# Kernel tuning notes

Measured on AMD Instinct MI355X. Metric: run time of the kernel, lower is better.

Reference implementation:

```python
import jax, jax.numpy as jnp
import numpy as np

N, E, S = 10000, 100000, 10            # nodes, edges, message-passing steps
NODE_F, EDGE_F, L, H, OUT = 30, 4, 128, 128, 3


def _mlp(h, W0, b0, W1, b1, W2, b2):
    # Linear->ReLU, Linear->ReLU, Linear (build_mlp with num_hidden_layers=2)
    h = jax.nn.relu(h @ W0 + b0)
    h = jax.nn.relu(h @ W1 + b1)
    return h @ W2 + b2


def _ln(h, g, b):
    # torch.nn.LayerNorm over last dim, eps=1e-5, biased variance
    m = h.mean(-1, keepdims=True)
    v = h.var(-1, keepdims=True)
    return (h - m) * jax.lax.rsqrt(v + 1e-5) * g + b


def setup_inputs():
    key = jax.random.key(0)
    ks = iter(jax.random.split(key, 64))

    def w(shape, fan):
        return jax.random.normal(next(ks), shape, dtype=jnp.float32) / np.float32(np.sqrt(fan))

    d = {}
    d["x"] = jax.random.normal(next(ks), (N, NODE_F), dtype=jnp.float32)
    d["ea"] = jax.random.normal(next(ks), (E, EDGE_F), dtype=jnp.float32)
    d["ei"] = jax.random.randint(next(ks), (2, E), 0, N)
    # encoder node ('en') / edge ('ee') MLP+LayerNorm params
    for pre, fin in (("en", NODE_F), ("ee", EDGE_F)):
        d[pre + "W0"] = w((fin, H), fin); d[pre + "b0"] = jnp.zeros((H,), jnp.float32)
        d[pre + "W1"] = w((H, H), H);     d[pre + "b1"] = jnp.zeros((H,), jnp.float32)
        d[pre + "W2"] = w((H, L), H);     d[pre + "b2"] = jnp.zeros((L,), jnp.float32)
        d[pre + "g"] = jnp.ones((L,), jnp.float32); d[pre + "bt"] = jnp.zeros((L,), jnp.float32)
    # processor edge ('pe', in=3L) / node ('pn', in=2L) params, stacked over S steps
    for pre, fin in (("pe", 3 * L), ("pn", 2 * L)):
        d[pre + "W0"] = w((S, fin, H), fin); d[pre + "b0"] = jnp.zeros((S, H), jnp.float32)
        d[pre + "W1"] = w((S, H, H), H);     d[pre + "b1"] = jnp.zeros((S, H), jnp.float32)
        d[pre + "W2"] = w((S, H, L), H);     d[pre + "b2"] = jnp.zeros((S, L), jnp.float32)
        d[pre + "g"] = jnp.ones((S, L), jnp.float32); d[pre + "bt"] = jnp.zeros((S, L), jnp.float32)
    # decoder MLP (no LayerNorm)
    d["dW0"] = w((L, H), L); d["db0"] = jnp.zeros((H,), jnp.float32)
    d["dW1"] = w((H, H), H); d["db1"] = jnp.zeros((H,), jnp.float32)
    d["dW2"] = w((H, OUT), H); d["db2"] = jnp.zeros((OUT,), jnp.float32)
    return d


def reference(x, ea, ei,
              enW0, enb0, enW1, enb1, enW2, enb2, eng, enbt,
              eeW0, eeb0, eeW1, eeb1, eeW2, eeb2, eeg, eebt,
              peW0, peb0, peW1, peb1, peW2, peb2, peg, pebt,
              pnW0, pnb0, pnW1, pnb1, pnW2, pnb2, png, pnbt,
              dW0, db0, dW1, db1, dW2, db2):
    src, dst = ei[0], ei[1]
    # encode (GraphIndependent)
    hx = _ln(_mlp(x, enW0, enb0, enW1, enb1, enW2, enb2), eng, enbt)   # [N, L]
    he = _ln(_mlp(ea, eeW0, eeb0, eeW1, eeb1, eeW2, eeb2), eeg, eebt)  # [E, L]

    # process: S InteractionNetwork steps with residuals
    def step(carry, p):
        cx, ce = carry
        (eW0, eb0, eW1, eb1, eW2, eb2, eg, ebt,
         nW0, nb0, nW1, nb1, nW2, nb2, ng, nbt) = p
        edge_in = jnp.concatenate([cx[src], cx[dst], ce], axis=-1)     # [E, 3L]
        ue = _ln(_mlp(edge_in, eW0, eb0, eW1, eb1, eW2, eb2), eg, ebt)  # [E, L]
        agg = jax.ops.segment_sum(ue, dst, num_segments=N)              # [N, L]
        un = _ln(_mlp(jnp.concatenate([cx, agg], axis=-1), nW0, nb0, nW1, nb1, nW2, nb2), ng, nbt)
        return (cx + un, ce + ue), None

    (hx, he), _ = jax.lax.scan(
        step, (hx, he),
        (peW0, peb0, peW1, peb1, peW2, peb2, peg, pebt,
         pnW0, pnb0, pnW1, pnb1, pnW2, pnb2, png, pnbt))

    # decode
    return _mlp(hx, dW0, db0, dW1, db1, dW2, db2)  # [N, OUT]
```

## Files before the change

### kernel.cpp

```cpp
#include <hip/hip_runtime.h>


#define NN 10000
#define NE 100000
#define STEPS 10
#define NODE_F 30
#define EDGE_F 4
#define L 128
#define AP 132
#define BP 36

#define WS_STRIDE 136
#define AB_STRIDE 136

typedef __bf16 bf16x8 __attribute__((ext_vector_type(8)));
typedef float f32x4 __attribute__((ext_vector_type(4)));

__device__ __forceinline__ unsigned short f2bf(float f) {
  __bf16 b = (__bf16)f;
  return __builtin_bit_cast(unsigned short, b);
}
__device__ __forceinline__ float bf2f(unsigned short u) {
  return __builtin_bit_cast(float, (unsigned)u << 16);
}


__device__ __forceinline__ void stage_W(unsigned short* __restrict__ Ws,
                                        const unsigned short* __restrict__ Wt,
                                        int K, int sec, int tid) {
#pragma unroll
  for (int p = 0; p < 8; ++p) {
    int u = tid + p * 256;
    int n = u >> 4, kk = u & 15;
    uint4 v = *(const uint4*)(Wt + (size_t)n * K + sec * 128 + kk * 8);
    *(uint4*)&Ws[n * WS_STRIDE + kk * 8] = v;
  }
}

__device__ __forceinline__ void init_acc(f32x4 acc[2][4], const float* __restrict__ b,
                                         int wcol, int l16) {
#pragma unroll
  for (int j = 0; j < 4; ++j) {
    float bv = b[wcol + j * 16 + l16];
#pragma unroll
    for (int i = 0; i < 2; ++i) acc[i][j] = f32x4{bv, bv, bv, bv};
  }
}

__device__ __forceinline__ void layer_gbf(const unsigned short* __restrict__ ap0,
                                          const unsigned short* __restrict__ ap1,
                                          const unsigned short* __restrict__ Ws,
                                          f32x4 acc[2][4], int wcol, int l4, int l16) {
#pragma unroll
  for (int kk = 0; kk < 4; ++kk) {
    bf16x8 af[2];
    af[0] = *(const bf16x8*)(ap0 + kk * 32 + l4 * 8);
    af[1] = *(const bf16x8*)(ap1 + kk * 32 + l4 * 8);
#pragma unroll
    for (int j = 0; j < 4; ++j) {
      bf16x8 bv = *(const bf16x8*)&Ws[(wcol + j * 16 + l16) * WS_STRIDE + kk * 32 + l4 * 8];
#pragma unroll
      for (int i = 0; i < 2; ++i)
        acc[i][j] = __builtin_amdgcn_mfma_f32_16x16x32_bf16(af[i], bv, acc[i][j], 0, 0, 0);
    }
  }
}

__device__ __forceinline__ void layer_lds(const unsigned short* __restrict__ Ab,
                                          const unsigned short* __restrict__ Ws,
                                          f32x4 acc[2][4], int wrow, int wcol, int l4, int l16) {
#pragma unroll
  for (int kk = 0; kk < 4; ++kk) {
    bf16x8 af[2];
#pragma unroll
    for (int i = 0; i < 2; ++i)
      af[i] = *(const bf16x8*)&Ab[(wrow + i * 16 + l16) * AB_STRIDE + kk * 32 + l4 * 8];
#pragma unroll
    for (int j = 0; j < 4; ++j) {
      bf16x8 bv = *(const bf16x8*)&Ws[(wcol + j * 16 + l16) * WS_STRIDE + kk * 32 + l4 * 8];
#pragma unroll
      for (int i = 0; i < 2; ++i)
        acc[i][j] = __builtin_amdgcn_mfma_f32_16x16x32_bf16(af[i], bv, acc[i][j], 0, 0, 0);
    }
  }
}

__device__ __forceinline__ void relu_to_Ab(unsigned short* __restrict__ Ab, f32x4 acc[2][4],
                                           int wrow, int wcol, int l4, int l16) {
#pragma unroll
  for (int i = 0; i < 2; ++i)
#pragma unroll
    for (int j = 0; j < 4; ++j)
#pragma unroll
      for (int r = 0; r < 4; ++r) {
        int row = wrow + i * 16 + l4 * 4 + r;
        int col = wcol + j * 16 + l16;
        __bf16 v = (__bf16)fmaxf(acc[i][j][r], 0.f);
        Ab[row * AB_STRIDE + col] = __builtin_bit_cast(unsigned short, v);
      }
}

__device__ __forceinline__ void ln_partials(const f32x4 acc[2][4], float ps[2][4], float ps2[2][4]) {
#pragma unroll
  for (int i = 0; i < 2; ++i)
#pragma unroll
    for (int r = 0; r < 4; ++r) {
      float s = 0.f, s2 = 0.f;
#pragma unroll
      for (int j = 0; j < 4; ++j) { float v = acc[i][j][r]; s += v; s2 += v * v; }
#pragma unroll
      for (int off = 1; off < 16; off <<= 1) {
        s += __shfl_xor(s, off, 64);
        s2 += __shfl_xor(s2, off, 64);
      }
      ps[i][r] = s; ps2[i][r] = s2;
    }
}


__global__ __launch_bounds__(256) void deg_kernel(const int* __restrict__ ei, int* __restrict__ cnt) {
  int e = blockIdx.x * 256 + threadIdx.x;
  if (e < NE) atomicAdd(&cnt[ei[NE + e]], 1);
}

__global__ __launch_bounds__(256) void scan_kernel(const int* __restrict__ cnt,
                                                   int* __restrict__ off, int* __restrict__ cur) {
  __shared__ int sums[256];
  int t = threadIdx.x;
  int base = t * 40;
  int local = 0;
  for (int i = 0; i < 40; ++i) { int n = base + i; if (n < NN) local += cnt[n]; }
  sums[t] = local;
  __syncthreads();
  int val = local;
  for (int d = 1; d < 256; d <<= 1) {
    int add = (t >= d) ? sums[t - d] : 0;
    __syncthreads();
    sums[t] += add;
    __syncthreads();
  }
  int run = sums[t] - val;
  for (int i = 0; i < 40; ++i) {
    int n = base + i;
    if (n < NN) { off[n] = run; cur[n] = run; run += cnt[n]; }
  }
  if (t == 255) off[NN] = sums[255];
}

__global__ __launch_bounds__(256) void scatter_kernel(const int* __restrict__ ei,
                                                      int* __restrict__ cur, int* __restrict__ eid) {
  int e = blockIdx.x * 256 + threadIdx.x;
  if (e < NE) { int p = atomicAdd(&cur[ei[NE + e]], 1); eid[p] = e; }
}

__global__ __launch_bounds__(256) void agg_kernel(const unsigned short* __restrict__ ue,
                                                  const int* __restrict__ off,
                                                  const int* __restrict__ eid,
                                                  unsigned short* __restrict__ agg) {
  int node = blockIdx.x * 4 + (threadIdx.x >> 6);
  if (node >= NN) return;
  int lane = threadIdx.x & 63;
  int c0 = lane * 2;
  int p0 = off[node], p1 = off[node + 1];
  float sx = 0.f, sy = 0.f;
  for (int p = p0; p < p1; ++p) {
    unsigned v = *(const unsigned*)&ue[(size_t)eid[p] * L + c0];
    sx += __builtin_bit_cast(float, v << 16);
    sy += __builtin_bit_cast(float, v & 0xffff0000u);
  }
  unsigned o = (unsigned)f2bf(sx) | ((unsigned)f2bf(sy) << 16);
  *(unsigned*)&agg[(size_t)node * L + c0] = o;
}


__global__ __launch_bounds__(256) void edge_step_mfma(
    const unsigned short* __restrict__ hx_bf, unsigned short* __restrict__ he_bf,
    unsigned short* __restrict__ ue_bf,
    const int* __restrict__ ei,
    const unsigned short* __restrict__ W0t, const float* __restrict__ b0,
    const unsigned short* __restrict__ W1t, const float* __restrict__ b1,
    const unsigned short* __restrict__ W2t, const float* __restrict__ b2,
    const float* __restrict__ g, const float* __restrict__ bt) {
  __shared__ __align__(16) unsigned short Ws[128 * WS_STRIDE];
  __shared__ __align__(16) unsigned short Ab[64 * AB_STRIDE];
  __shared__ int sidx[64], didx[64];
  int tid = threadIdx.x;
  int w = tid >> 6, lane = tid & 63;
  int l4 = lane >> 4, l16 = lane & 15;
  int wrow = (w >> 1) * 32, wcol = (w & 1) * 64;
  int e0 = blockIdx.x * 64;
  if (tid < 64) {
    int e = min(e0 + tid, NE - 1);
    sidx[tid] = ei[e];
    didx[tid] = ei[NE + e];
  }
  f32x4 acc[2][4];
  init_acc(acc, b0, wcol, l16);
  __syncthreads();
  for (int sec = 0; sec < 3; ++sec) {
    stage_W(Ws, W0t, 384, sec, tid);
    const unsigned short* ap[2];
#pragma unroll
    for (int i = 0; i < 2; ++i) {
      int r = wrow + i * 16 + l16;
      if (sec == 0)      ap[i] = hx_bf + (size_t)sidx[r] * L;
      else if (sec == 1) ap[i] = hx_bf + (size_t)didx[r] * L;
      else               ap[i] = he_bf + (size_t)min(e0 + r, NE - 1) * L;
    }
    __syncthreads();
    layer_gbf(ap[0], ap[1], Ws, acc, wcol, l4, l16);
    __syncthreads();
  }
  relu_to_Ab(Ab, acc, wrow, wcol, l4, l16);
  stage_W(Ws, W1t, 128, 0, tid);
  init_acc(acc, b1, wcol, l16);
  __syncthreads();
  layer_lds(Ab, Ws, acc, wrow, wcol, l4, l16);
  __syncthreads();
  relu_to_Ab(Ab, acc, wrow, wcol, l4, l16);
  stage_W(Ws, W2t, 128, 0, tid);
  init_acc(acc, b2, wcol, l16);
  __syncthreads();
  layer_lds(Ab, Ws, acc, wrow, wcol, l4, l16);
  float ps[2][4], ps2[2][4];
  ln_partials(acc, ps, ps2);
  __syncthreads();
  float* red = (float*)Ab;
  if (l16 == 0) {
#pragma unroll
    for (int i = 0; i < 2; ++i)
#pragma unroll
      for (int r = 0; r < 4; ++r) {
        int row = wrow + i * 16 + l4 * 4 + r;
        red[(w & 1) * 128 + row * 2 + 0] = ps[i][r];
        red[(w & 1) * 128 + row * 2 + 1] = ps2[i][r];
      }
  }
  __syncthreads();
  float gv[4], btv[4];
#pragma unroll
  for (int j = 0; j < 4; ++j) {
    int col = wcol + j * 16 + l16;
    gv[j] = g[col]; btv[j] = bt[col];
  }
#pragma unroll
  for (int i = 0; i < 2; ++i)
#pragma unroll
    for (int r = 0; r < 4; ++r) {
      int row = wrow + i * 16 + l4 * 4 + r;
      float s  = red[row * 2]     + red[128 + row * 2];
      float s2 = red[row * 2 + 1] + red[128 + row * 2 + 1];
      float m = s * (1.f / 128.f);
      float inv = rsqrtf(s2 * (1.f / 128.f) - m * m + 1e-5f);
      int e = e0 + row;
      if (e < NE) {
        size_t hoff = (size_t)e * L;
#pragma unroll
        for (int j = 0; j < 4; ++j) {
          int col = wcol + j * 16 + l16;
          float u = (acc[i][j][r] - m) * inv * gv[j] + btv[j];
          unsigned short old = he_bf[hoff + col];
          he_bf[hoff + col] = f2bf(bf2f(old) + u);
          ue_bf[hoff + col] = f2bf(u);
        }
      }
    }
}

__global__ __launch_bounds__(256) void node_step_mfma(
    float* __restrict__ hx, unsigned short* __restrict__ hx_bf,
    const unsigned short* __restrict__ agg_bf,
    const unsigned short* __restrict__ W0t, const float* __restrict__ b0,
    const unsigned short* __restrict__ W1t, const float* __restrict__ b1,
    const unsigned short* __restrict__ W2t, const float* __restrict__ b2,
    const float* __restrict__ g, const float* __restrict__ bt) {
  __shared__ __align__(16) unsigned short Ws[128 * WS_STRIDE];
  __shared__ __align__(16) unsigned short Ab[64 * AB_STRIDE];
  int tid = threadIdx.x;
  int w = tid >> 6, lane = tid & 63;
  int l4 = lane >> 4, l16 = lane & 15;
  int wrow = (w >> 1) * 32, wcol = (w & 1) * 64;
  int n0 = blockIdx.x * 64;
  f32x4 acc[2][4];
  init_acc(acc, b0, wcol, l16);
  for (int sec = 0; sec < 2; ++sec) {
    __syncthreads();
    stage_W(Ws, W0t, 256, sec, tid);
    const unsigned short* base = (sec == 0) ? hx_bf : agg_bf;
    const unsigned short* ap[2];
#pragma unroll
    for (int i = 0; i < 2; ++i)
      ap[i] = base + (size_t)min(n0 + wrow + i * 16 + l16, NN - 1) * L;
    __syncthreads();
    layer_gbf(ap[0], ap[1], Ws, acc, wcol, l4, l16);
  }
  __syncthreads();
  relu_to_Ab(Ab, acc, wrow, wcol, l4, l16);
  stage_W(Ws, W1t, 128, 0, tid);
  init_acc(acc, b1, wcol, l16);
  __syncthreads();
  layer_lds(Ab, Ws, acc, wrow, wcol, l4, l16);
  __syncthreads();
  relu_to_Ab(Ab, acc, wrow, wcol, l4, l16);
  stage_W(Ws, W2t, 128, 0, tid);
  init_acc(acc, b2, wcol, l16);
  __syncthreads();
  layer_lds(Ab, Ws, acc, wrow, wcol, l4, l16);
  float ps[2][4], ps2[2][4];
  ln_partials(acc, ps, ps2);
  __syncthreads();
  float* red = (float*)Ab;
  if (l16 == 0) {
#pragma unroll
    for (int i = 0; i < 2; ++i)
#pragma unroll
      for (int r = 0; r < 4; ++r) {
        int row = wrow + i * 16 + l4 * 4 + r;
        red[(w & 1) * 128 + row * 2 + 0] = ps[i][r];
        red[(w & 1) * 128 + row * 2 + 1] = ps2[i][r];
      }
  }
  __syncthreads();
  float gv[4], btv[4];
#pragma unroll
  for (int j = 0; j < 4; ++j) {
    int col = wcol + j * 16 + l16;
    gv[j] = g[col]; btv[j] = bt[col];
  }
#pragma unroll
  for (int i = 0; i < 2; ++i)
#pragma unroll
    for (int r = 0; r < 4; ++r) {
      int row = wrow + i * 16 + l4 * 4 + r;
      float s  = red[row * 2]     + red[128 + row * 2];
      float s2 = red[row * 2 + 1] + red[128 + row * 2 + 1];
      float m = s * (1.f / 128.f);
      float inv = rsqrtf(s2 * (1.f / 128.f) - m * m + 1e-5f);
      int n = n0 + row;
      if (n < NN) {
#pragma unroll
        for (int j = 0; j < 4; ++j) {
          int col = wcol + j * 16 + l16;
          float un = (acc[i][j][r] - m) * inv * gv[j] + btv[j];
          float nv = hx[(size_t)n * L + col] + un;
          hx[(size_t)n * L + col] = nv;
          hx_bf[(size_t)n * L + col] = f2bf(nv);
        }
      }
    }
}

__global__ __launch_bounds__(256) void enc_edge_mfma(
    const float* __restrict__ ea,
    const float* __restrict__ W0, const float* __restrict__ b0,
    const unsigned short* __restrict__ W1t, const float* __restrict__ b1,
    const unsigned short* __restrict__ W2t, const float* __restrict__ b2,
    const float* __restrict__ g, const float* __restrict__ bt,
    unsigned short* __restrict__ he_bf) {
  __shared__ __align__(16) unsigned short Ws[128 * WS_STRIDE];
  __shared__ __align__(16) unsigned short Ab[64 * AB_STRIDE];
  int tid = threadIdx.x;
  int w = tid >> 6, lane = tid & 63;
  int l4 = lane >> 4, l16 = lane & 15;
  int wrow = (w >> 1) * 32, wcol = (w & 1) * 64;
  int e0 = blockIdx.x * 64;
  {
    int row = tid >> 2, cbase = (tid & 3) * 32;
    int e = min(e0 + row, NE - 1);
    float4 eav = *(const float4*)&ea[(size_t)e * 4];
#pragma unroll
    for (int c = 0; c < 32; ++c) {
      int col = cbase + c;
      float sum = b0[col] + eav.x * W0[col] + eav.y * W0[128 + col] +
                  eav.z * W0[256 + col] + eav.w * W0[384 + col];
      __bf16 v = (__bf16)fmaxf(sum, 0.f);
      Ab[row * AB_STRIDE + col] = __builtin_bit_cast(unsigned short, v);
    }
  }
  stage_W(Ws, W1t, 128, 0, tid);
  f32x4 acc[2][4];
  init_acc(acc, b1, wcol, l16);
  __syncthreads();
  layer_lds(Ab, Ws, acc, wrow, wcol, l4, l16);
  __syncthreads();
  relu_to_Ab(Ab, acc, wrow, wcol, l4, l16);
  stage_W(Ws, W2t, 128, 0, tid);
  init_acc(acc, b2, wcol, l16);
  __syncthreads();
  layer_lds(Ab, Ws, acc, wrow, wcol, l4, l16);
  float ps[2][4], ps2[2][4];
  ln_partials(acc, ps, ps2);
  __syncthreads();
  float* red = (float*)Ab;
  if (l16 == 0) {
#pragma unroll
    for (int i = 0; i < 2; ++i)
#pragma unroll
      for (int r = 0; r < 4; ++r) {
        int row = wrow + i * 16 + l4 * 4 + r;
        red[(w & 1) * 128 + row * 2 + 0] = ps[i][r];
        red[(w & 1) * 128 + row * 2 + 1] = ps2[i][r];
      }
  }
  __syncthreads();
  float gv[4], btv[4];
#pragma unroll
  for (int j = 0; j < 4; ++j) {
    int col = wcol + j * 16 + l16;
    gv[j] = g[col]; btv[j] = bt[col];
  }
#pragma unroll
  for (int i = 0; i < 2; ++i)
#pragma unroll
    for (int r = 0; r < 4; ++r) {
      int row = wrow + i * 16 + l4 * 4 + r;
      float s  = red[row * 2]     + red[128 + row * 2];
      float s2 = red[row * 2 + 1] + red[128 + row * 2 + 1];
      float m = s * (1.f / 128.f);
      float inv = rsqrtf(s2 * (1.f / 128.f) - m * m + 1e-5f);
      int e = e0 + row;
      if (e < NE) {
#pragma unroll
        for (int j = 0; j < 4; ++j) {
          int col = wcol + j * 16 + l16;
          he_bf[(size_t)e * L + col] = f2bf((acc[i][j][r] - m) * inv * gv[j] + btv[j]);
        }
      }
    }
}


__global__ __launch_bounds__(256) void wprep_kernel(
    const float* __restrict__ W0, const float* __restrict__ W1, const float* __restrict__ W2,
    unsigned short* __restrict__ out, int K0, int steps) {
  int per_step = 128 * (K0 + 256);
  int idx = blockIdx.x * 256 + threadIdx.x;
  if (idx >= steps * per_step) return;
  int s = idx / per_step, r = idx - s * per_step;
  float v;
  if (r < 128 * K0) {
    int n = r / K0, k = r - n * K0;
    v = W0[(size_t)s * K0 * 128 + (size_t)k * 128 + n];
  } else {
    r -= 128 * K0;
    const float* W = (r < 16384) ? W1 : W2;
    r &= 16383;
    int n = r >> 7, k = r & 127;
    v = W[(size_t)s * 16384 + k * 128 + n];
  }
  out[idx] = f2bf(v);
}

__global__ __launch_bounds__(256) void tprep_kernel(
    const float* __restrict__ W1, const float* __restrict__ W2, unsigned short* __restrict__ out) {
  int idx = blockIdx.x * 256 + threadIdx.x;
  const float* W = (idx < 16384) ? W1 : W2;
  int r = idx & 16383;
  int n = r >> 7, k = r & 127;
  out[idx] = f2bf(W[k * 128 + n]);
}


__device__ __forceinline__ void load_B(float* __restrict__ Bs, const float* __restrict__ W,
                                       int K, int k0, int tid) {
#pragma unroll
  for (int p = 0; p < 16; ++p) {
    int idx = tid + p * 256;
    int kk = idx >> 7;
    int c = idx & 127;
    float v = 0.f;
    if (k0 + kk < K) v = W[(size_t)(k0 + kk) * L + c];
    Bs[c * BP + kk] = v;
  }
}

__device__ __forceinline__ void fma32(const float* __restrict__ As, const float* __restrict__ Bs,
                                      float acc[4][8], int ty, int tx, int koff) {
#pragma unroll
  for (int kk = 0; kk < 32; kk += 4) {
    float4 a[4];
    float4 b[8];
#pragma unroll
    for (int i = 0; i < 4; ++i)
      a[i] = *(const float4*)&As[(ty + 16 * i) * AP + koff + kk];
#pragma unroll
    for (int j = 0; j < 8; ++j)
      b[j] = *(const float4*)&Bs[(tx + 16 * j) * BP + kk];
#pragma unroll
    for (int i = 0; i < 4; ++i)
#pragma unroll
      for (int j = 0; j < 8; ++j) {
        acc[i][j] = fmaf(a[i].x, b[j].x, acc[i][j]);
        acc[i][j] = fmaf(a[i].y, b[j].y, acc[i][j]);
        acc[i][j] = fmaf(a[i].z, b[j].z, acc[i][j]);
        acc[i][j] = fmaf(a[i].w, b[j].w, acc[i][j]);
      }
  }
}

__device__ __forceinline__ void init_bias(float acc[4][8], const float* __restrict__ b, int tx) {
#pragma unroll
  for (int j = 0; j < 8; ++j) {
    float bv = b[tx + 16 * j];
#pragma unroll
    for (int i = 0; i < 4; ++i) acc[i][j] = bv;
  }
}

__device__ __forceinline__ void store_relu(float* __restrict__ As, float acc[4][8], int ty, int tx) {
#pragma unroll
  for (int i = 0; i < 4; ++i)
#pragma unroll
    for (int j = 0; j < 8; ++j)
      As[(ty + 16 * i) * AP + tx + 16 * j] = fmaxf(acc[i][j], 0.f);
}

__device__ __forceinline__ void layer_As(const float* __restrict__ As, float* __restrict__ Bs,
                                         const float* __restrict__ W, const float* __restrict__ bias,
                                         int K, float acc[4][8], int tid, int ty, int tx) {
  init_bias(acc, bias, tx);
  int nc = (K + 31) >> 5;
  for (int bc = 0; bc < nc; ++bc) {
    __syncthreads();
    load_B(Bs, W, K, bc * 32, tid);
    __syncthreads();
    fma32(As, Bs, acc, ty, tx, bc * 32);
  }
}

__device__ __forceinline__ void fillA_gather(float* __restrict__ As, const float* __restrict__ base,
                                             const int* __restrict__ ridx, int tid) {
#pragma unroll
  for (int p = 0; p < 8; ++p) {
    int idx = tid + p * 256;
    int r = idx >> 5;
    int c4 = idx & 31;
    float4 v = *(const float4*)&base[(size_t)ridx[r] * L + c4 * 4];
    *(float4*)&As[r * AP + c4 * 4] = v;
  }
}

__device__ __forceinline__ void lnorm(float acc[4][8], const float* __restrict__ g,
                                      const float* __restrict__ bt, int tx) {
  float gv[8], bv[8];
#pragma unroll
  for (int j = 0; j < 8; ++j) { gv[j] = g[tx + 16 * j]; bv[j] = bt[tx + 16 * j]; }
#pragma unroll
  for (int i = 0; i < 4; ++i) {
    float s = 0.f, s2 = 0.f;
#pragma unroll
    for (int j = 0; j < 8; ++j) { s += acc[i][j]; s2 += acc[i][j] * acc[i][j]; }
#pragma unroll
    for (int off = 1; off < 16; off <<= 1) {
      s  += __shfl_xor(s, off, 64);
      s2 += __shfl_xor(s2, off, 64);
    }
    float m = s * (1.f / 128.f);
    float var = s2 * (1.f / 128.f) - m * m;
    float inv = rsqrtf(var + 1e-5f);
#pragma unroll
    for (int j = 0; j < 8; ++j) acc[i][j] = (acc[i][j] - m) * inv * gv[j] + bv[j];
  }
}

__global__ __launch_bounds__(256) void enc_node_kernel(
    const float* __restrict__ x,
    const float* __restrict__ W0, const float* __restrict__ b0,
    const float* __restrict__ W1, const float* __restrict__ b1,
    const float* __restrict__ W2, const float* __restrict__ b2,
    const float* __restrict__ g, const float* __restrict__ bt,
    float* __restrict__ hx, unsigned short* __restrict__ hx_bf) {
  __shared__ float As[64 * AP];
  __shared__ float Bs[128 * BP];
  int tid = threadIdx.x, ty = tid >> 4, tx = tid & 15;
  int n0 = blockIdx.x * 64;
#pragma unroll
  for (int p = 0; p < 8; ++p) {
    int idx = tid + p * 256;
    int r = idx >> 5, c = idx & 31;
    int n = min(n0 + r, NN - 1);
    As[r * AP + c] = (c < NODE_F) ? x[(size_t)n * NODE_F + c] : 0.f;
  }
  float acc[4][8];
  init_bias(acc, b0, tx);
  __syncthreads();
  load_B(Bs, W0, NODE_F, 0, tid);
  __syncthreads();
  fma32(As, Bs, acc, ty, tx, 0);

  __syncthreads(); store_relu(As, acc, ty, tx);
  layer_As(As, Bs, W1, b1, L, acc, tid, ty, tx);
  __syncthreads(); store_relu(As, acc, ty, tx);
  layer_As(As, Bs, W2, b2, L, acc, tid, ty, tx);
  lnorm(acc, g, bt, tx);
#pragma unroll
  for (int i = 0; i < 4; ++i) {
    int n = n0 + ty + 16 * i;
    if (n < NN)
#pragma unroll
      for (int j = 0; j < 8; ++j) {
        float v = acc[i][j];
        hx[(size_t)n * L + tx + 16 * j] = v;
        hx_bf[(size_t)n * L + tx + 16 * j] = f2bf(v);
      }
  }
}

__global__ __launch_bounds__(256) void dec_kernel(
    const float* __restrict__ hx,
    const float* __restrict__ W0, const float* __restrict__ b0,
    const float* __restrict__ W1, const float* __restrict__ b1,
    const float* __restrict__ W2, const float* __restrict__ b2,
    float* __restrict__ out) {
  __shared__ float As[64 * AP];
  __shared__ float Bs[128 * BP];
  __shared__ int nidx[64];
  int tid = threadIdx.x, ty = tid >> 4, tx = tid & 15;
  int n0 = blockIdx.x * 64;
  if (tid < 64) nidx[tid] = min(n0 + tid, NN - 1);
  __syncthreads();
  fillA_gather(As, hx, nidx, tid);
  float acc[4][8];
  layer_As(As, Bs, W0, b0, L, acc, tid, ty, tx);
  __syncthreads(); store_relu(As, acc, ty, tx);
  layer_As(As, Bs, W1, b1, L, acc, tid, ty, tx);
  __syncthreads(); store_relu(As, acc, ty, tx);
  __syncthreads();
  if (tid < 192) {
    int r = tid / 3, o = tid - (tid / 3) * 3;
    int n = n0 + r;
    if (n < NN) {
      float s = b2[o];
#pragma unroll 8
      for (int k = 0; k < L; ++k) s = fmaf(As[r * AP + k], W2[k * 3 + o], s);
      out[(size_t)n * 3 + o] = s;
    }
  }
}


extern "C" void kernel_launch(void* const* d_in, const int* in_sizes, int n_in,
                              void* d_out, int out_size, void* d_ws, size_t ws_size,
                              hipStream_t stream) {
  (void)in_sizes; (void)n_in; (void)out_size; (void)ws_size;
  const float* x    = (const float*)d_in[0];
  const float* ea   = (const float*)d_in[1];
  const int*   ei   = (const int*)d_in[2];
  const float* enW0 = (const float*)d_in[3];  const float* enb0 = (const float*)d_in[4];
  const float* enW1 = (const float*)d_in[5];  const float* enb1 = (const float*)d_in[6];
  const float* enW2 = (const float*)d_in[7];  const float* enb2 = (const float*)d_in[8];
  const float* eng  = (const float*)d_in[9];  const float* enbt = (const float*)d_in[10];
  const float* eeW0 = (const float*)d_in[11]; const float* eeb0 = (const float*)d_in[12];
  const float* eeW1 = (const float*)d_in[13]; const float* eeb1 = (const float*)d_in[14];
  const float* eeW2 = (const float*)d_in[15]; const float* eeb2 = (const float*)d_in[16];
  const float* eeg  = (const float*)d_in[17]; const float* eebt = (const float*)d_in[18];
  const float* peW0 = (const float*)d_in[19]; const float* peb0 = (const float*)d_in[20];
  const float* peW1 = (const float*)d_in[21]; const float* peb1 = (const float*)d_in[22];
  const float* peW2 = (const float*)d_in[23]; const float* peb2 = (const float*)d_in[24];
  const float* peg  = (const float*)d_in[25]; const float* pebt = (const float*)d_in[26];
  const float* pnW0 = (const float*)d_in[27]; const float* pnb0 = (const float*)d_in[28];
  const float* pnW1 = (const float*)d_in[29]; const float* pnb1 = (const float*)d_in[30];
  const float* pnW2 = (const float*)d_in[31]; const float* pnb2 = (const float*)d_in[32];
  const float* png  = (const float*)d_in[33]; const float* pnbt = (const float*)d_in[34];
  const float* dW0  = (const float*)d_in[35]; const float* db0  = (const float*)d_in[36];
  const float* dW1  = (const float*)d_in[37]; const float* db1  = (const float*)d_in[38];
  const float* dW2  = (const float*)d_in[39]; const float* db2  = (const float*)d_in[40];

  const size_t F_HX = (size_t)NN * L, F_HE = (size_t)NE * L;
  const size_t W_PE = 819200, W_PN = 655360, W_EE = 32768;

  float* hx = (float*)d_ws;
  unsigned short* he_bf  = (unsigned short*)(hx + F_HX);
  unsigned short* ue_bf  = he_bf + F_HE;
  unsigned short* hx_bf  = ue_bf + F_HE;
  unsigned short* agg_bf = hx_bf + F_HX;
  unsigned short* wt_pe  = agg_bf + F_HX;
  unsigned short* wt_pn  = wt_pe + W_PE;
  unsigned short* wt_ee  = wt_pn + W_PN;
  int* cnt = (int*)(wt_ee + W_EE);
  int* off = cnt + NN;
  int* cur = off + NN + 1;
  int* eid = cur + NN;

  dim3 blk(256);
  int grid_n = (NN + 63) / 64;
  int grid_e = (NE + 63) / 64;

  wprep_kernel<<<(10 * 81920 + 255) / 256, blk, 0, stream>>>(peW0, peW1, peW2, wt_pe, 384, 10);
  wprep_kernel<<<(10 * 65536 + 255) / 256, blk, 0, stream>>>(pnW0, pnW1, pnW2, wt_pn, 256, 10);
  tprep_kernel<<<128, blk, 0, stream>>>(eeW1, eeW2, wt_ee);

  hipMemsetAsync(cnt, 0, (size_t)NN * 4, stream);
  deg_kernel<<<(NE + 255) / 256, blk, 0, stream>>>(ei, cnt);
  scan_kernel<<<1, blk, 0, stream>>>(cnt, off, cur);
  scatter_kernel<<<(NE + 255) / 256, blk, 0, stream>>>(ei, cur, eid);

  enc_node_kernel<<<grid_n, blk, 0, stream>>>(x, enW0, enb0, enW1, enb1, enW2, enb2, eng, enbt, hx, hx_bf);
  enc_edge_mfma<<<grid_e, blk, 0, stream>>>(ea, eeW0, eeb0, wt_ee, eeb1, wt_ee + 16384, eeb2, eeg, eebt, he_bf);

  for (int s = 0; s < STEPS; ++s) {
    const unsigned short* pe = wt_pe + (size_t)s * 81920;
    const unsigned short* pn = wt_pn + (size_t)s * 65536;
    edge_step_mfma<<<grid_e, blk, 0, stream>>>(
        hx_bf, he_bf, ue_bf, ei,
        pe,                 peb0 + (size_t)s * L,
        pe + 49152,         peb1 + (size_t)s * L,
        pe + 49152 + 16384, peb2 + (size_t)s * L,
        peg + (size_t)s * L, pebt + (size_t)s * L);
    agg_kernel<<<(NN + 3) / 4, blk, 0, stream>>>(ue_bf, off, eid, agg_bf);
    node_step_mfma<<<grid_n, blk, 0, stream>>>(
        hx, hx_bf, agg_bf,
        pn,                 pnb0 + (size_t)s * L,
        pn + 32768,         pnb1 + (size_t)s * L,
        pn + 32768 + 16384, pnb2 + (size_t)s * L,
        png + (size_t)s * L, pnbt + (size_t)s * L);
  }

  dec_kernel<<<grid_n, blk, 0, stream>>>(hx, dW0, db0, dW1, db1, dW2, db2, (float*)d_out);
}
```

Baseline: 995.8 us.

## Fuse edge aggregation into node kernel and enlarge edge tiles with prefetched weights

```diff
diff --git a/kernel.cpp b/kernel.cpp
--- a/kernel.cpp
+++ b/kernel.cpp
@@ -25,6 +25,24 @@
 }
 
 
+__device__ __forceinline__ void wload8(uint4 wr[8], const unsigned short* __restrict__ Wt,
+                                       int K, int koff, int tid) {
+#pragma unroll
+  for (int p = 0; p < 8; ++p) {
+    int u = tid + p * 256;
+    int n = u >> 4, kk = u & 15;
+    wr[p] = *(const uint4*)(Wt + (size_t)n * K + koff + kk * 8);
+  }
+}
+__device__ __forceinline__ void wstore8(const uint4 wr[8], unsigned short* __restrict__ Ws, int tid) {
+#pragma unroll
+  for (int p = 0; p < 8; ++p) {
+    int u = tid + p * 256;
+    int n = u >> 4, kk = u & 15;
+    *(uint4*)&Ws[n * WS_STRIDE + kk * 8] = wr[p];
+  }
+}
+
 __device__ __forceinline__ void stage_W(unsigned short* __restrict__ Ws,
                                         const unsigned short* __restrict__ Wt,
                                         int K, int sec, int tid) {
@@ -37,6 +55,76 @@
   }
 }
 
+
+__device__ __forceinline__ void layer_gbf4(const unsigned short* const ap[4],
+                                           const unsigned short* __restrict__ Ws,
+                                           f32x4 acc[4][4], int wcol, int l4, int l16) {
+#pragma unroll
+  for (int kk = 0; kk < 4; ++kk) {
+    bf16x8 af[4];
+#pragma unroll
+    for (int i = 0; i < 4; ++i)
+      af[i] = *(const bf16x8*)(ap[i] + kk * 32 + l4 * 8);
+#pragma unroll
+    for (int j = 0; j < 4; ++j) {
+      bf16x8 bv = *(const bf16x8*)&Ws[(wcol + j * 16 + l16) * WS_STRIDE + kk * 32 + l4 * 8];
+#pragma unroll
+      for (int i = 0; i < 4; ++i)
+        acc[i][j] = __builtin_amdgcn_mfma_f32_16x16x32_bf16(af[i], bv, acc[i][j], 0, 0, 0);
+    }
+  }
+}
+
+__device__ __forceinline__ void layer_lds4(const unsigned short* __restrict__ Ab,
+                                           const unsigned short* __restrict__ Ws,
+                                           f32x4 acc[4][4], int wrow, int wcol, int l4, int l16) {
+#pragma unroll
+  for (int kk = 0; kk < 4; ++kk) {
+    bf16x8 af[4];
+#pragma unroll
+    for (int i = 0; i < 4; ++i)
+      af[i] = *(const bf16x8*)&Ab[(wrow + i * 16 + l16) * AB_STRIDE + kk * 32 + l4 * 8];
+#pragma unroll
+    for (int j = 0; j < 4; ++j) {
+      bf16x8 bv = *(const bf16x8*)&Ws[(wcol + j * 16 + l16) * WS_STRIDE + kk * 32 + l4 * 8];
+#pragma unroll
+      for (int i = 0; i < 4; ++i)
+        acc[i][j] = __builtin_amdgcn_mfma_f32_16x16x32_bf16(af[i], bv, acc[i][j], 0, 0, 0);
+    }
+  }
+}
+
+__device__ __forceinline__ void relu_to_Ab4(unsigned short* __restrict__ Ab, f32x4 acc[4][4],
+                                            int wrow, int wcol, int l4, int l16) {
+#pragma unroll
+  for (int i = 0; i < 4; ++i)
+#pragma unroll
+    for (int j = 0; j < 4; ++j)
+#pragma unroll
+      for (int r = 0; r < 4; ++r) {
+        int row = wrow + i * 16 + l4 * 4 + r;
+        int col = wcol + j * 16 + l16;
+        Ab[row * AB_STRIDE + col] = f2bf(fmaxf(acc[i][j][r], 0.f));
+      }
+}
+
+__device__ __forceinline__ void ln_partials4(const f32x4 acc[4][4], float ps[4][4], float ps2[4][4]) {
+#pragma unroll
+  for (int i = 0; i < 4; ++i)
+#pragma unroll
+    for (int r = 0; r < 4; ++r) {
+      float s = 0.f, s2 = 0.f;
+#pragma unroll
+      for (int j = 0; j < 4; ++j) { float v = acc[i][j][r]; s += v; s2 += v * v; }
+#pragma unroll
+      for (int off = 1; off < 16; off <<= 1) {
+        s += __shfl_xor(s, off, 64);
+        s2 += __shfl_xor(s2, off, 64);
+      }
+      ps[i][r] = s; ps2[i][r] = s2;
+    }
+}
+
 __device__ __forceinline__ void init_acc(f32x4 acc[2][4], const float* __restrict__ b,
                                          int wcol, int l16) {
 #pragma unroll
@@ -95,8 +183,7 @@
       for (int r = 0; r < 4; ++r) {
         int row = wrow + i * 16 + l4 * 4 + r;
         int col = wcol + j * 16 + l16;
-        __bf16 v = (__bf16)fmaxf(acc[i][j][r], 0.f);
-        Ab[row * AB_STRIDE + col] = __builtin_bit_cast(unsigned short, v);
+        Ab[row * AB_STRIDE + col] = f2bf(fmaxf(acc[i][j][r], 0.f));
       }
 }
 
@@ -151,25 +238,6 @@
                                                       int* __restrict__ cur, int* __restrict__ eid) {
   int e = blockIdx.x * 256 + threadIdx.x;
   if (e < NE) { int p = atomicAdd(&cur[ei[NE + e]], 1); eid[p] = e; }
-}
-
-__global__ __launch_bounds__(256) void agg_kernel(const unsigned short* __restrict__ ue,
-                                                  const int* __restrict__ off,
-                                                  const int* __restrict__ eid,
-                                                  unsigned short* __restrict__ agg) {
-  int node = blockIdx.x * 4 + (threadIdx.x >> 6);
-  if (node >= NN) return;
-  int lane = threadIdx.x & 63;
-  int c0 = lane * 2;
-  int p0 = off[node], p1 = off[node + 1];
-  float sx = 0.f, sy = 0.f;
-  for (int p = p0; p < p1; ++p) {
-    unsigned v = *(const unsigned*)&ue[(size_t)eid[p] * L + c0];
-    sx += __builtin_bit_cast(float, v << 16);
-    sy += __builtin_bit_cast(float, v & 0xffff0000u);
-  }
-  unsigned o = (unsigned)f2bf(sx) | ((unsigned)f2bf(sy) << 16);
-  *(unsigned*)&agg[(size_t)node * L + c0] = o;
 }
 
 
@@ -182,74 +250,108 @@
     const unsigned short* __restrict__ W2t, const float* __restrict__ b2,
     const float* __restrict__ g, const float* __restrict__ bt) {
   __shared__ __align__(16) unsigned short Ws[128 * WS_STRIDE];
-  __shared__ __align__(16) unsigned short Ab[64 * AB_STRIDE];
-  __shared__ int sidx[64], didx[64];
+  __shared__ __align__(16) unsigned short Ab[128 * AB_STRIDE];
+  __shared__ int sidx[128], didx[128];
   int tid = threadIdx.x;
   int w = tid >> 6, lane = tid & 63;
   int l4 = lane >> 4, l16 = lane & 15;
-  int wrow = (w >> 1) * 32, wcol = (w & 1) * 64;
-  int e0 = blockIdx.x * 64;
-  if (tid < 64) {
+  int wrow = (w >> 1) * 64, wcol = (w & 1) * 64;
+  int e0 = blockIdx.x * 128;
+
+  uint4 wr[8];
+  wload8(wr, W0t, 384, 0, tid);
+  if (tid < 128) {
     int e = min(e0 + tid, NE - 1);
     sidx[tid] = ei[e];
     didx[tid] = ei[NE + e];
   }
-  f32x4 acc[2][4];
-  init_acc(acc, b0, wcol, l16);
-  __syncthreads();
-  for (int sec = 0; sec < 3; ++sec) {
-    stage_W(Ws, W0t, 384, sec, tid);
-    const unsigned short* ap[2];
-#pragma unroll
-    for (int i = 0; i < 2; ++i) {
-      int r = wrow + i * 16 + l16;
-      if (sec == 0)      ap[i] = hx_bf + (size_t)sidx[r] * L;
-      else if (sec == 1) ap[i] = hx_bf + (size_t)didx[r] * L;
-      else               ap[i] = he_bf + (size_t)min(e0 + r, NE - 1) * L;
-    }
-    __syncthreads();
-    layer_gbf(ap[0], ap[1], Ws, acc, wcol, l4, l16);
-    __syncthreads();
-  }
-  relu_to_Ab(Ab, acc, wrow, wcol, l4, l16);
-  stage_W(Ws, W1t, 128, 0, tid);
-  init_acc(acc, b1, wcol, l16);
-  __syncthreads();
-  layer_lds(Ab, Ws, acc, wrow, wcol, l4, l16);
-  __syncthreads();
-  relu_to_Ab(Ab, acc, wrow, wcol, l4, l16);
-  stage_W(Ws, W2t, 128, 0, tid);
-  init_acc(acc, b2, wcol, l16);
-  __syncthreads();
-  layer_lds(Ab, Ws, acc, wrow, wcol, l4, l16);
-  float ps[2][4], ps2[2][4];
-  ln_partials(acc, ps, ps2);
+  float bv0[4], bv1[4], bv2[4], gv[4], btv[4];
+#pragma unroll
+  for (int j = 0; j < 4; ++j) {
+    int c = wcol + j * 16 + l16;
+    bv0[j] = b0[c]; bv1[j] = b1[c]; bv2[j] = b2[c]; gv[j] = g[c]; btv[j] = bt[c];
+  }
+  f32x4 acc[4][4];
+#pragma unroll
+  for (int j = 0; j < 4; ++j) {
+    f32x4 b = {bv0[j], bv0[j], bv0[j], bv0[j]};
+#pragma unroll
+    for (int i = 0; i < 4; ++i) acc[i][j] = b;
+  }
+  wstore8(wr, Ws, tid);
+  __syncthreads();
+  wload8(wr, W0t, 384, 128, tid);
+  {
+    const unsigned short* ap[4];
+#pragma unroll
+    for (int i = 0; i < 4; ++i) ap[i] = hx_bf + (size_t)sidx[wrow + i * 16 + l16] * L;
+    layer_gbf4(ap, Ws, acc, wcol, l4, l16);
+  }
+  __syncthreads();
+  wstore8(wr, Ws, tid);
+  __syncthreads();
+  wload8(wr, W0t, 384, 256, tid);
+  {
+    const unsigned short* ap[4];
+#pragma unroll
+    for (int i = 0; i < 4; ++i) ap[i] = hx_bf + (size_t)didx[wrow + i * 16 + l16] * L;
+    layer_gbf4(ap, Ws, acc, wcol, l4, l16);
+  }
+  __syncthreads();
+  wstore8(wr, Ws, tid);
+  __syncthreads();
+  wload8(wr, W1t, 128, 0, tid);
+  {
+    const unsigned short* ap[4];
+#pragma unroll
+    for (int i = 0; i < 4; ++i) ap[i] = he_bf + (size_t)min(e0 + wrow + i * 16 + l16, NE - 1) * L;
+    layer_gbf4(ap, Ws, acc, wcol, l4, l16);
+  }
+  relu_to_Ab4(Ab, acc, wrow, wcol, l4, l16);
+  __syncthreads();
+  wstore8(wr, Ws, tid);
+  __syncthreads();
+  wload8(wr, W2t, 128, 0, tid);
+#pragma unroll
+  for (int j = 0; j < 4; ++j) {
+    f32x4 b = {bv1[j], bv1[j], bv1[j], bv1[j]};
+#pragma unroll
+    for (int i = 0; i < 4; ++i) acc[i][j] = b;
+  }
+  layer_lds4(Ab, Ws, acc, wrow, wcol, l4, l16);
+  __syncthreads();
+  wstore8(wr, Ws, tid);
+  relu_to_Ab4(Ab, acc, wrow, wcol, l4, l16);
+  __syncthreads();
+#pragma unroll
+  for (int j = 0; j < 4; ++j) {
+    f32x4 b = {bv2[j], bv2[j], bv2[j], bv2[j]};
+#pragma unroll
+    for (int i = 0; i < 4; ++i) acc[i][j] = b;
+  }
+  layer_lds4(Ab, Ws, acc, wrow, wcol, l4, l16);
+  float ps[4][4], ps2[4][4];
+  ln_partials4(acc, ps, ps2);
   __syncthreads();
   float* red = (float*)Ab;
   if (l16 == 0) {
 #pragma unroll
-    for (int i = 0; i < 2; ++i)
+    for (int i = 0; i < 4; ++i)
 #pragma unroll
       for (int r = 0; r < 4; ++r) {
         int row = wrow + i * 16 + l4 * 4 + r;
-        red[(w & 1) * 128 + row * 2 + 0] = ps[i][r];
-        red[(w & 1) * 128 + row * 2 + 1] = ps2[i][r];
-      }
-  }
-  __syncthreads();
-  float gv[4], btv[4];
-#pragma unroll
-  for (int j = 0; j < 4; ++j) {
-    int col = wcol + j * 16 + l16;
-    gv[j] = g[col]; btv[j] = bt[col];
-  }
-#pragma unroll
-  for (int i = 0; i < 2; ++i)
+        red[(w & 1) * 256 + row * 2 + 0] = ps[i][r];
+        red[(w & 1) * 256 + row * 2 + 1] = ps2[i][r];
+      }
+  }
+  __syncthreads();
+#pragma unroll
+  for (int i = 0; i < 4; ++i)
 #pragma unroll
     for (int r = 0; r < 4; ++r) {
       int row = wrow + i * 16 + l4 * 4 + r;
-      float s  = red[row * 2]     + red[128 + row * 2];
-      float s2 = red[row * 2 + 1] + red[128 + row * 2 + 1];
+      float s  = red[row * 2]     + red[256 + row * 2];
+      float s2 = red[row * 2 + 1] + red[256 + row * 2 + 1];
       float m = s * (1.f / 128.f);
       float inv = rsqrtf(s2 * (1.f / 128.f) - m * m + 1e-5f);
       int e = e0 + row;
@@ -267,33 +369,69 @@
     }
 }
 
+
 __global__ __launch_bounds__(256) void node_step_mfma(
     float* __restrict__ hx, unsigned short* __restrict__ hx_bf,
-    const unsigned short* __restrict__ agg_bf,
+    const unsigned short* __restrict__ ue_bf,
+    const int* __restrict__ off, const int* __restrict__ eid,
     const unsigned short* __restrict__ W0t, const float* __restrict__ b0,
     const unsigned short* __restrict__ W1t, const float* __restrict__ b1,
     const unsigned short* __restrict__ W2t, const float* __restrict__ b2,
     const float* __restrict__ g, const float* __restrict__ bt) {
   __shared__ __align__(16) unsigned short Ws[128 * WS_STRIDE];
   __shared__ __align__(16) unsigned short Ab[64 * AB_STRIDE];
+  __shared__ __align__(16) unsigned short Ag[64 * AB_STRIDE];
   int tid = threadIdx.x;
   int w = tid >> 6, lane = tid & 63;
   int l4 = lane >> 4, l16 = lane & 15;
   int wrow = (w >> 1) * 32, wcol = (w & 1) * 64;
   int n0 = blockIdx.x * 64;
+  {
+    int r = tid >> 2;
+    int cseg = (tid & 3) * 32;
+    int n = n0 + r;
+    float a[32];
+#pragma unroll
+    for (int q = 0; q < 32; ++q) a[q] = 0.f;
+    if (n < NN) {
+      int p0 = off[n], p1 = off[n + 1];
+      for (int p = p0; p < p1; ++p) {
+        const unsigned short* row = ue_bf + (size_t)eid[p] * L + cseg;
+#pragma unroll
+        for (int q = 0; q < 4; ++q) {
+          uint4 v = *(const uint4*)(row + q * 8);
+          a[q * 8 + 0] += __builtin_bit_cast(float, v.x << 16);
+          a[q * 8 + 1] += __builtin_bit_cast(float, v.x & 0xffff0000u);
+          a[q * 8 + 2] += __builtin_bit_cast(float, v.y << 16);
+          a[q * 8 + 3] += __builtin_bit_cast(float, v.y & 0xffff0000u);
+          a[q * 8 + 4] += __builtin_bit_cast(float, v.z << 16);
+          a[q * 8 + 5] += __builtin_bit_cast(float, v.z & 0xffff0000u);
+          a[q * 8 + 6] += __builtin_bit_cast(float, v.w << 16);
+          a[q * 8 + 7] += __builtin_bit_cast(float, v.w & 0xffff0000u);
+        }
+      }
+    }
+#pragma unroll
+    for (int q = 0; q < 16; ++q) {
+      unsigned o = (unsigned)f2bf(a[2 * q]) | ((unsigned)f2bf(a[2 * q + 1]) << 16);
+      *(unsigned*)&Ag[r * AB_STRIDE + cseg + 2 * q] = o;
+    }
+  }
+  stage_W(Ws, W0t, 256, 0, tid);
   f32x4 acc[2][4];
   init_acc(acc, b0, wcol, l16);
-  for (int sec = 0; sec < 2; ++sec) {
-    __syncthreads();
-    stage_W(Ws, W0t, 256, sec, tid);
-    const unsigned short* base = (sec == 0) ? hx_bf : agg_bf;
+  __syncthreads();
+  {
     const unsigned short* ap[2];
 #pragma unroll
     for (int i = 0; i < 2; ++i)
-      ap[i] = base + (size_t)min(n0 + wrow + i * 16 + l16, NN - 1) * L;
-    __syncthreads();
+      ap[i] = hx_bf + (size_t)min(n0 + wrow + i * 16 + l16, NN - 1) * L;
     layer_gbf(ap[0], ap[1], Ws, acc, wcol, l4, l16);
   }
+  __syncthreads();
+  stage_W(Ws, W0t, 256, 1, tid);
+  __syncthreads();
+  layer_lds(Ag, Ws, acc, wrow, wcol, l4, l16);
   __syncthreads();
   relu_to_Ab(Ab, acc, wrow, wcol, l4, l16);
   stage_W(Ws, W1t, 128, 0, tid);
@@ -349,6 +487,7 @@
       }
     }
 }
+
 
 __global__ __launch_bounds__(256) void enc_edge_mfma(
     const float* __restrict__ ea,
@@ -373,8 +512,7 @@
       int col = cbase + c;
       float sum = b0[col] + eav.x * W0[col] + eav.y * W0[128 + col] +
                   eav.z * W0[256 + col] + eav.w * W0[384 + col];
-      __bf16 v = (__bf16)fmaxf(sum, 0.f);
-      Ab[row * AB_STRIDE + col] = __builtin_bit_cast(unsigned short, v);
+      Ab[row * AB_STRIDE + col] = f2bf(fmaxf(sum, 0.f));
     }
   }
   stage_W(Ws, W1t, 128, 0, tid);
@@ -673,8 +811,7 @@
   unsigned short* he_bf  = (unsigned short*)(hx + F_HX);
   unsigned short* ue_bf  = he_bf + F_HE;
   unsigned short* hx_bf  = ue_bf + F_HE;
-  unsigned short* agg_bf = hx_bf + F_HX;
-  unsigned short* wt_pe  = agg_bf + F_HX;
+  unsigned short* wt_pe  = hx_bf + F_HX;
   unsigned short* wt_pn  = wt_pe + W_PE;
   unsigned short* wt_ee  = wt_pn + W_PN;
   int* cnt = (int*)(wt_ee + W_EE);
@@ -683,8 +820,9 @@
   int* eid = cur + NN;
 
   dim3 blk(256);
-  int grid_n = (NN + 63) / 64;
-  int grid_e = (NE + 63) / 64;
+  int grid_n  = (NN + 63) / 64;
+  int grid_e64  = (NE + 63) / 64;
+  int grid_e128 = (NE + 127) / 128;
 
   wprep_kernel<<<(10 * 81920 + 255) / 256, blk, 0, stream>>>(peW0, peW1, peW2, wt_pe, 384, 10);
   wprep_kernel<<<(10 * 65536 + 255) / 256, blk, 0, stream>>>(pnW0, pnW1, pnW2, wt_pn, 256, 10);
@@ -696,20 +834,19 @@
   scatter_kernel<<<(NE + 255) / 256, blk, 0, stream>>>(ei, cur, eid);
 
   enc_node_kernel<<<grid_n, blk, 0, stream>>>(x, enW0, enb0, enW1, enb1, enW2, enb2, eng, enbt, hx, hx_bf);
-  enc_edge_mfma<<<grid_e, blk, 0, stream>>>(ea, eeW0, eeb0, wt_ee, eeb1, wt_ee + 16384, eeb2, eeg, eebt, he_bf);
+  enc_edge_mfma<<<grid_e64, blk, 0, stream>>>(ea, eeW0, eeb0, wt_ee, eeb1, wt_ee + 16384, eeb2, eeg, eebt, he_bf);
 
   for (int s = 0; s < STEPS; ++s) {
     const unsigned short* pe = wt_pe + (size_t)s * 81920;
     const unsigned short* pn = wt_pn + (size_t)s * 65536;
-    edge_step_mfma<<<grid_e, blk, 0, stream>>>(
+    edge_step_mfma<<<grid_e128, blk, 0, stream>>>(
         hx_bf, he_bf, ue_bf, ei,
         pe,                 peb0 + (size_t)s * L,
         pe + 49152,         peb1 + (size_t)s * L,
         pe + 49152 + 16384, peb2 + (size_t)s * L,
         peg + (size_t)s * L, pebt + (size_t)s * L);
-    agg_kernel<<<(NN + 3) / 4, blk, 0, stream>>>(ue_bf, off, eid, agg_bf);
     node_step_mfma<<<grid_n, blk, 0, stream>>>(
-        hx, hx_bf, agg_bf,
+        hx, hx_bf, ue_bf, off, eid,
         pn,                 pnb0 + (size_t)s * L,
         pn + 32768,         pnb1 + (size_t)s * L,
         pn + 32768 + 16384, pnb2 + (size_t)s * L,
```

Result: slower. 1.387 ms (+39.3%).

## Fuse CSR segment-sum aggregation into node step kernel via LDS

Applied to the files above, without the earlier changes.

```diff
diff --git a/kernel.cpp b/kernel.cpp
--- a/kernel.cpp
+++ b/kernel.cpp
@@ -37,6 +37,7 @@
   }
 }
 
+
 __device__ __forceinline__ void init_acc(f32x4 acc[2][4], const float* __restrict__ b,
                                          int wcol, int l16) {
 #pragma unroll
@@ -95,8 +96,7 @@
       for (int r = 0; r < 4; ++r) {
         int row = wrow + i * 16 + l4 * 4 + r;
         int col = wcol + j * 16 + l16;
-        __bf16 v = (__bf16)fmaxf(acc[i][j][r], 0.f);
-        Ab[row * AB_STRIDE + col] = __builtin_bit_cast(unsigned short, v);
+        Ab[row * AB_STRIDE + col] = f2bf(fmaxf(acc[i][j][r], 0.f));
       }
 }
 
@@ -151,25 +151,6 @@
                                                       int* __restrict__ cur, int* __restrict__ eid) {
   int e = blockIdx.x * 256 + threadIdx.x;
   if (e < NE) { int p = atomicAdd(&cur[ei[NE + e]], 1); eid[p] = e; }
-}
-
-__global__ __launch_bounds__(256) void agg_kernel(const unsigned short* __restrict__ ue,
-                                                  const int* __restrict__ off,
-                                                  const int* __restrict__ eid,
-                                                  unsigned short* __restrict__ agg) {
-  int node = blockIdx.x * 4 + (threadIdx.x >> 6);
-  if (node >= NN) return;
-  int lane = threadIdx.x & 63;
-  int c0 = lane * 2;
-  int p0 = off[node], p1 = off[node + 1];
-  float sx = 0.f, sy = 0.f;
-  for (int p = p0; p < p1; ++p) {
-    unsigned v = *(const unsigned*)&ue[(size_t)eid[p] * L + c0];
-    sx += __builtin_bit_cast(float, v << 16);
-    sy += __builtin_bit_cast(float, v & 0xffff0000u);
-  }
-  unsigned o = (unsigned)f2bf(sx) | ((unsigned)f2bf(sy) << 16);
-  *(unsigned*)&agg[(size_t)node * L + c0] = o;
 }
 
 
@@ -267,33 +248,69 @@
     }
 }
 
+
 __global__ __launch_bounds__(256) void node_step_mfma(
     float* __restrict__ hx, unsigned short* __restrict__ hx_bf,
-    const unsigned short* __restrict__ agg_bf,
+    const unsigned short* __restrict__ ue_bf,
+    const int* __restrict__ off, const int* __restrict__ eid,
     const unsigned short* __restrict__ W0t, const float* __restrict__ b0,
     const unsigned short* __restrict__ W1t, const float* __restrict__ b1,
     const unsigned short* __restrict__ W2t, const float* __restrict__ b2,
     const float* __restrict__ g, const float* __restrict__ bt) {
   __shared__ __align__(16) unsigned short Ws[128 * WS_STRIDE];
   __shared__ __align__(16) unsigned short Ab[64 * AB_STRIDE];
+  __shared__ __align__(16) unsigned short Ag[64 * AB_STRIDE];
   int tid = threadIdx.x;
   int w = tid >> 6, lane = tid & 63;
   int l4 = lane >> 4, l16 = lane & 15;
   int wrow = (w >> 1) * 32, wcol = (w & 1) * 64;
   int n0 = blockIdx.x * 64;
+  {
+    int r = tid >> 2;
+    int cseg = (tid & 3) * 32;
+    int n = n0 + r;
+    float a[32];
+#pragma unroll
+    for (int q = 0; q < 32; ++q) a[q] = 0.f;
+    if (n < NN) {
+      int p0 = off[n], p1 = off[n + 1];
+      for (int p = p0; p < p1; ++p) {
+        const unsigned short* row = ue_bf + (size_t)eid[p] * L + cseg;
+#pragma unroll
+        for (int q = 0; q < 4; ++q) {
+          uint4 v = *(const uint4*)(row + q * 8);
+          a[q * 8 + 0] += __builtin_bit_cast(float, v.x << 16);
+          a[q * 8 + 1] += __builtin_bit_cast(float, v.x & 0xffff0000u);
+          a[q * 8 + 2] += __builtin_bit_cast(float, v.y << 16);
+          a[q * 8 + 3] += __builtin_bit_cast(float, v.y & 0xffff0000u);
+          a[q * 8 + 4] += __builtin_bit_cast(float, v.z << 16);
+          a[q * 8 + 5] += __builtin_bit_cast(float, v.z & 0xffff0000u);
+          a[q * 8 + 6] += __builtin_bit_cast(float, v.w << 16);
+          a[q * 8 + 7] += __builtin_bit_cast(float, v.w & 0xffff0000u);
+        }
+      }
+    }
+#pragma unroll
+    for (int q = 0; q < 16; ++q) {
+      unsigned o = (unsigned)f2bf(a[2 * q]) | ((unsigned)f2bf(a[2 * q + 1]) << 16);
+      *(unsigned*)&Ag[r * AB_STRIDE + cseg + 2 * q] = o;
+    }
+  }
+  stage_W(Ws, W0t, 256, 0, tid);
   f32x4 acc[2][4];
   init_acc(acc, b0, wcol, l16);
-  for (int sec = 0; sec < 2; ++sec) {
-    __syncthreads();
-    stage_W(Ws, W0t, 256, sec, tid);
-    const unsigned short* base = (sec == 0) ? hx_bf : agg_bf;
+  __syncthreads();
+  {
     const unsigned short* ap[2];
 #pragma unroll
     for (int i = 0; i < 2; ++i)
-      ap[i] = base + (size_t)min(n0 + wrow + i * 16 + l16, NN - 1) * L;
-    __syncthreads();
+      ap[i] = hx_bf + (size_t)min(n0 + wrow + i * 16 + l16, NN - 1) * L;
     layer_gbf(ap[0], ap[1], Ws, acc, wcol, l4, l16);
   }
+  __syncthreads();
+  stage_W(Ws, W0t, 256, 1, tid);
+  __syncthreads();
+  layer_lds(Ag, Ws, acc, wrow, wcol, l4, l16);
   __syncthreads();
   relu_to_Ab(Ab, acc, wrow, wcol, l4, l16);
   stage_W(Ws, W1t, 128, 0, tid);
@@ -349,6 +366,7 @@
       }
     }
 }
+
 
 __global__ __launch_bounds__(256) void enc_edge_mfma(
     const float* __restrict__ ea,
@@ -373,8 +391,7 @@
       int col = cbase + c;
       float sum = b0[col] + eav.x * W0[col] + eav.y * W0[128 + col] +
                   eav.z * W0[256 + col] + eav.w * W0[384 + col];
-      __bf16 v = (__bf16)fmaxf(sum, 0.f);
-      Ab[row * AB_STRIDE + col] = __builtin_bit_cast(unsigned short, v);
+      Ab[row * AB_STRIDE + col] = f2bf(fmaxf(sum, 0.f));
     }
   }
   stage_W(Ws, W1t, 128, 0, tid);
@@ -673,8 +690,7 @@
   unsigned short* he_bf  = (unsigned short*)(hx + F_HX);
   unsigned short* ue_bf  = he_bf + F_HE;
   unsigned short* hx_bf  = ue_bf + F_HE;
-  unsigned short* agg_bf = hx_bf + F_HX;
-  unsigned short* wt_pe  = agg_bf + F_HX;
+  unsigned short* wt_pe  = hx_bf + F_HX;
   unsigned short* wt_pn  = wt_pe + W_PE;
   unsigned short* wt_ee  = wt_pn + W_PN;
   int* cnt = (int*)(wt_ee + W_EE);
@@ -707,9 +723,8 @@
         pe + 49152,         peb1 + (size_t)s * L,
         pe + 49152 + 16384, peb2 + (size_t)s * L,
         peg + (size_t)s * L, pebt + (size_t)s * L);
-    agg_kernel<<<(NN + 3) / 4, blk, 0, stream>>>(ue_bf, off, eid, agg_bf);
     node_step_mfma<<<grid_n, blk, 0, stream>>>(
-        hx, hx_bf, agg_bf,
+        hx, hx_bf, ue_bf, off, eid,
         pn,                 pnb0 + (size_t)s * L,
         pn + 32768,         pnb1 + (size_t)s * L,
         pn + 32768 + 16384, pnb2 + (size_t)s * L,
```

New measurement: 947.7 us. 4.8% less time.
